# Performance work log

Measured on AMD Instinct MI355X. Metric: run time of the kernel, lower is better.

The kernel has to match this reference:

```python
import jax, jax.numpy as jnp
import numpy as np

T = 35        # points per voxel
D, H, W = 10, 400, 352  # voxel grid (KITTI car setting)
EPS = 1e-5    # BatchNorm eps


def setup_inputs() -> dict:
    key = jax.random.key(0)
    ks = jax.random.split(key, 10)
    K = 15000  # non-empty voxels in the frame
    feature = jax.random.normal(ks[0], (K, T, 7), jnp.float32)
    # realistic padding: each voxel has 5..35 valid points, rest zero
    npts = jax.random.randint(ks[1], (K,), 5, T + 1)
    valid = jnp.arange(T)[None, :] < npts[:, None]
    feature = feature * valid[:, :, None].astype(jnp.float32)
    c_b = jnp.zeros((K, 1), jnp.int32)
    c_d = jax.random.randint(ks[2], (K, 1), 0, D).astype(jnp.int32)
    c_h = jax.random.randint(ks[3], (K, 1), 0, H).astype(jnp.int32)
    c_w = jax.random.randint(ks[4], (K, 1), 0, W).astype(jnp.int32)
    coordinate = jnp.concatenate([c_b, c_d, c_h, c_w], axis=1)
    W1 = jax.random.normal(ks[5], (7, 16), jnp.float32) * 0.1
    b1 = jnp.zeros((16,), jnp.float32)
    g1 = jnp.ones((16,), jnp.float32)
    be1 = jnp.zeros((16,), jnp.float32)
    W2 = jax.random.normal(ks[6], (32, 64), jnp.float32) * 0.1
    b2 = jnp.zeros((64,), jnp.float32)
    g2 = jnp.ones((64,), jnp.float32)
    be2 = jnp.zeros((64,), jnp.float32)
    return {"feature": feature, "coordinate": coordinate, "bs": 1,
            "W1": W1, "b1": b1, "g1": g1, "be1": be1,
            "W2": W2, "b2": b2, "g2": g2, "be2": be2}


def _vfe(x, mask, Wm, b, g, be):
    # Linear + ReLU per point: [K, T, cin] -> [K, T, cmid]
    pw = jax.nn.relu(jnp.einsum('ktc,cd->ktd', x, Wm) + b)
    # BatchNorm1d (training mode): per-channel stats over (K, T), biased var
    mu = pw.mean(axis=(0, 1))
    var = pw.var(axis=(0, 1))
    pw = (pw - mu) * jax.lax.rsqrt(var + EPS) * g + be
    # max over points, broadcast-concat (VoxelNet VFE)
    agg = pw.max(axis=1, keepdims=True)               # [K, 1, cmid]
    cat = jnp.concatenate([pw, jnp.broadcast_to(agg, pw.shape)], axis=-1)
    return cat * mask  # mask padded points


def reference(feature, coordinate, bs, W1, b1, g1, be1, W2, b2, g2, be2):
    # mask: point is valid if its channel-wise max != 0 (as in original)
    vmax = feature.max(axis=2, keepdims=True)          # [K, T, 1]
    mask = (vmax != 0).astype(feature.dtype)
    x = _vfe(feature, mask, W1, b1, g1, be1)           # [K, T, 32]
    x = _vfe(x, mask, W2, b2, g2, be2)                 # [K, T, 128]
    voxelwise = x.max(axis=1)                          # [K, 128]
    # scatter into dense grid (sparse COO -> to_dense sums duplicates)
    out = jnp.zeros((bs, D, H, W, 128), feature.dtype)
    out = out.at[coordinate[:, 0], coordinate[:, 1],
                 coordinate[:, 2], coordinate[:, 3]].add(voxelwise)
    return out
```

## Files before the change

kernel.cpp:

```cpp
#include <hip/hip_runtime.h>
#include <math.h>

#define KVOX 15000
#define TP 35
#define CIN 7
#define CM1 16
#define CM2 64
#define NPTS (KVOX * TP)
#define DD 10
#define HH 400
#define WWID 352
#define NCELL (DD * HH * WWID)
#define EPSBN 1e-5f
#define NB1 256
#define NBV 3750

typedef float vfloat4 __attribute__((ext_vector_type(4)));
typedef int   vint4   __attribute__((ext_vector_type(4)));

#define NT4 (NCELL / 4)
__global__ __launch_bounds__(256) void init_kernel(vint4* __restrict__ table4)
{
    int i = blockIdx.x * 256 + threadIdx.x;
    table4[i] = (vint4){0x7FFFFFFF, 0x7FFFFFFF, 0x7FFFFFFF, 0x7FFFFFFF};
}

__global__ __launch_bounds__(256) void stats1_kernel(
    const float* __restrict__ feat, const int* __restrict__ coord,
    const float* __restrict__ W1, const float* __restrict__ b1,
    float* __restrict__ partial1, int* __restrict__ table)
{
    __shared__ float w1s[CIN * CM1];
    __shared__ float b1s[CM1];
    __shared__ float red[4][32];
    int tid = threadIdx.x;
    if (tid < CIN * CM1) w1s[tid] = W1[tid];
    if (tid < CM1) b1s[tid] = b1[tid];

    int g = blockIdx.x * 256 + tid;
    if (g < KVOX) {
        int cell = (coord[g * 4 + 1] * HH + coord[g * 4 + 2]) * WWID + coord[g * 4 + 3];
        atomicMin(&table[cell], g);
    }
    __syncthreads();

    float s[CM1], q[CM1];
#pragma unroll
    for (int c = 0; c < CM1; ++c) { s[c] = 0.f; q[c] = 0.f; }

    for (int i = blockIdx.x * 256 + tid; i < NPTS; i += NB1 * 256) {
        float f[CIN];
#pragma unroll
        for (int j = 0; j < CIN; ++j) f[j] = feat[(size_t)i * CIN + j];
#pragma unroll
        for (int c = 0; c < CM1; ++c) {
            float acc = b1s[c];
#pragma unroll
            for (int j = 0; j < CIN; ++j) acc = fmaf(f[j], w1s[j * CM1 + c], acc);
            float pw = fmaxf(acc, 0.f);
            s[c] += pw; q[c] += pw * pw;
        }
    }
#pragma unroll
    for (int c = 0; c < CM1; ++c) {
#pragma unroll
        for (int off = 32; off > 0; off >>= 1) {
            s[c] += __shfl_xor(s[c], off);
            q[c] += __shfl_xor(q[c], off);
        }
    }
    int wid = tid >> 6, lane = tid & 63;
    if (lane == 0) {
#pragma unroll
        for (int c = 0; c < CM1; ++c) { red[wid][c] = s[c]; red[wid][CM1 + c] = q[c]; }
    }
    __syncthreads();
    if (tid < 32)
        partial1[blockIdx.x * 32 + tid] =
            red[0][tid] + red[1][tid] + red[2][tid] + red[3][tid];
}

__global__ __launch_bounds__(256) void reduce1_kernel(
    const float* __restrict__ partial1, const float* __restrict__ g1,
    const float* __restrict__ be1, float* __restrict__ coef1)
{
    __shared__ float acc[8][32];
    __shared__ float tot[32];
    int tid = threadIdx.x;
    int c = tid & 31, part = tid >> 5;
    float v = 0.f;
    for (int b = part; b < NB1; b += 8) v += partial1[b * 32 + c];
    acc[part][c] = v;
    __syncthreads();
    if (tid < 32) {
        float t = 0.f;
#pragma unroll
        for (int p = 0; p < 8; ++p) t += acc[p][tid];
        tot[tid] = t;
    }
    __syncthreads();
    if (tid < CM1) {
        float inv = 1.f / (float)NPTS;
        float mu = tot[tid] * inv;
        float var = tot[CM1 + tid] * inv - mu * mu;
        float a = g1[tid] * rsqrtf(var + EPSBN);
        coef1[tid] = a;
        coef1[CM1 + tid] = be1[tid] - mu * a;
    }
}

__global__ __launch_bounds__(256) void vfe_once_kernel(
    const float* __restrict__ feat,
    const float* __restrict__ W1g, const float* __restrict__ b1g,
    const float* __restrict__ coef1,
    const float* __restrict__ W2g, const float* __restrict__ b2g,
    float* __restrict__ partial2,
    float* __restrict__ ext,
    int*   __restrict__ flags,
    vfloat4* __restrict__ compact4)
{
    __shared__ float sfeat[4][TP * CIN + 11];
    alignas(16) __shared__ float scat[4][TP * 32];
    __shared__ float smask[4][TP + 5];
    __shared__ float red2[4][2 * CM2];

    int tid = threadIdx.x, wid = tid >> 6, lane = tid & 63;
    int k = blockIdx.x * 4 + wid;
    int tg = lane >> 4, c1 = lane & 15;

    float w1r[CIN];
#pragma unroll
    for (int j = 0; j < CIN; ++j) w1r[j] = W1g[j * CM1 + c1];
    float b1r = b1g[c1];
    float a1r = coef1[c1], d1r = coef1[CM1 + c1];
    float w2r[32];
#pragma unroll
    for (int j = 0; j < 32; ++j) w2r[j] = W2g[j * CM2 + lane];
    float b2r = b2g[lane];

    float* F = sfeat[wid];
    float* CT = scat[wid];
    float* M = smask[wid];

    for (int i = lane; i < TP * CIN; i += 64)
        F[i] = feat[(size_t)k * (TP * CIN) + i];
    __syncthreads();

    float maxv = -INFINITY;
#pragma unroll
    for (int it = 0; it < 9; ++it) {
        int t = tg + 4 * it;
        if (t < TP) {
            float fv0 = F[t * CIN];
            float m7 = fv0;
            float acc = fmaf(fv0, w1r[0], b1r);
#pragma unroll
            for (int j = 1; j < CIN; ++j) {
                float fv = F[t * CIN + j];
                m7 = fmaxf(m7, fv);
                acc = fmaf(fv, w1r[j], acc);
            }
            float maskv = (m7 != 0.f) ? 1.f : 0.f;
            float pw = fmaxf(acc, 0.f);
            float bn = fmaf(pw, a1r, d1r);
            maxv = fmaxf(maxv, bn);
            CT[t * 32 + c1] = bn * maskv;
            if (c1 == 0) M[t] = maskv;
        }
    }
    maxv = fmaxf(maxv, __shfl_xor(maxv, 16));
    maxv = fmaxf(maxv, __shfl_xor(maxv, 32));
#pragma unroll
    for (int it = 0; it < 9; ++it) {
        int t = tg + 4 * it;
        if (t < TP) CT[t * 32 + 16 + c1] = maxv * M[t];
    }

    float s_acc = 0.f, q_acc = 0.f;
    float pwmax_v = -INFINITY, pwmin_v = INFINITY;
    float pwmax_a = -INFINITY, pwmin_a = INFINITY;
    float mmin = 1.f;
    for (int t = 0; t < TP; ++t) {
        const float4* r4 = reinterpret_cast<const float4*>(&CT[t * 32]);
        float acc0 = b2r, acc1 = 0.f;
#pragma unroll
        for (int i = 0; i < 8; i += 2) {
            float4 va = r4[i], vb = r4[i + 1];
            acc0 = fmaf(va.x, w2r[4 * i + 0], acc0);
            acc0 = fmaf(va.y, w2r[4 * i + 1], acc0);
            acc0 = fmaf(va.z, w2r[4 * i + 2], acc0);
            acc0 = fmaf(va.w, w2r[4 * i + 3], acc0);
            acc1 = fmaf(vb.x, w2r[4 * i + 4], acc1);
            acc1 = fmaf(vb.y, w2r[4 * i + 5], acc1);
            acc1 = fmaf(vb.z, w2r[4 * i + 6], acc1);
            acc1 = fmaf(vb.w, w2r[4 * i + 7], acc1);
        }
        float pw = fmaxf(acc0 + acc1, 0.f);
        s_acc += pw; q_acc += pw * pw;
        float mk = M[t];
        mmin = fminf(mmin, mk);
        pwmax_a = fmaxf(pwmax_a, pw);
        pwmin_a = fminf(pwmin_a, pw);
        pwmax_v = fmaxf(pwmax_v, (mk != 0.f) ? pw : -INFINITY);
        pwmin_v = fminf(pwmin_v, (mk != 0.f) ? pw : INFINITY);
    }

    float* E = ext + (size_t)k * 256;
    E[lane] = pwmax_v; E[64 + lane] = pwmin_v;
    E[128 + lane] = pwmax_a; E[192 + lane] = pwmin_a;
    if (lane == 0) flags[k] = (mmin == 0.f) ? 1 : 0;

    red2[wid][lane] = s_acc;
    red2[wid][CM2 + lane] = q_acc;
    __syncthreads();
    if (tid < 2 * CM2)
        partial2[(size_t)blockIdx.x * (2 * CM2) + tid] =
            red2[0][tid] + red2[1][tid] + red2[2][tid] + red2[3][tid];

    if (tid < 128)
        compact4[(size_t)blockIdx.x * 128 + tid] = (vfloat4){0.f, 0.f, 0.f, 0.f};
}

__global__ __launch_bounds__(256) void reduce2_kernel(
    const float* __restrict__ partial2, const float* __restrict__ g2,
    const float* __restrict__ be2, float* __restrict__ coef2)
{
    __shared__ float sred[4][2];
    int c = blockIdx.x;
    int tid = threadIdx.x;
    float s = 0.f, q = 0.f;
    for (int r = tid; r < NBV; r += 256) {
        s += partial2[(size_t)r * 128 + c];
        q += partial2[(size_t)r * 128 + CM2 + c];
    }
#pragma unroll
    for (int off = 32; off > 0; off >>= 1) {
        s += __shfl_xor(s, off);
        q += __shfl_xor(q, off);
    }
    int wid = tid >> 6;
    if ((tid & 63) == 0) { sred[wid][0] = s; sred[wid][1] = q; }
    __syncthreads();
    if (tid == 0) {
        float S = sred[0][0] + sred[1][0] + sred[2][0] + sred[3][0];
        float Q = sred[0][1] + sred[1][1] + sred[2][1] + sred[3][1];
        float inv = 1.f / (float)NPTS;
        float mu = S * inv;
        float var = Q * inv - mu * mu;
        float a = g2[c] * rsqrtf(var + EPSBN);
        coef2[c] = a;
        coef2[CM2 + c] = be2[c] - mu * a;
    }
}

__global__ __launch_bounds__(256) void finalize_kernel(
    const float* __restrict__ ext, const int* __restrict__ flags,
    const int* __restrict__ coord, const float* __restrict__ coef2,
    const int* __restrict__ table, float* __restrict__ compact)
{
    int tid = threadIdx.x;
    int k = blockIdx.x * 2 + (tid >> 7);
    int sub = tid & 127;
    int c = sub & 63, half = sub >> 6;
    float a = coef2[c], d = coef2[CM2 + c];
    const float* E = ext + (size_t)k * 256 + half * 128;
    float hi = E[c], lo = E[64 + c];
    float val = (a >= 0.f) ? fmaf(a, hi, d) : fmaf(a, lo, d);
    if (flags[k]) val = fmaxf(val, 0.f);
    int cell = (coord[k * 4 + 1] * HH + coord[k * 4 + 2]) * WWID + coord[k * 4 + 3];
    int w = table[cell];
    atomicAdd(&compact[(size_t)w * 128 + sub], val);
}

#define NBW (NCELL * 32 / 256)
__global__ __launch_bounds__(256) void write_kernel(
    vfloat4* __restrict__ out, const int* __restrict__ table,
    const vfloat4* __restrict__ compact4)
{
    int i = blockIdx.x * 256 + threadIdx.x;
    int cell = i >> 5;
    int w = table[cell];
    vfloat4 v = {0.f, 0.f, 0.f, 0.f};
    if (w < KVOX) v = compact4[w * 32 + (i & 31)];
    out[i] = v;
}

extern "C" void kernel_launch(void* const* d_in, const int* in_sizes, int n_in,
                              void* d_out, int out_size, void* d_ws, size_t ws_size,
                              hipStream_t stream)
{
    const float* feat = (const float*)d_in[0];
    const int*   coord = (const int*)d_in[1];
    const float* W1  = (const float*)d_in[3];
    const float* b1  = (const float*)d_in[4];
    const float* g1  = (const float*)d_in[5];
    const float* be1 = (const float*)d_in[6];
    const float* W2  = (const float*)d_in[7];
    const float* b2  = (const float*)d_in[8];
    const float* g2  = (const float*)d_in[9];
    const float* be2 = (const float*)d_in[10];
    float* out = (float*)d_out;

    int*   table    = (int*)d_ws;
    float* compact  = (float*)d_ws + NCELL;
    float* ext      = compact + (size_t)KVOX * 128;
    float* partial1 = ext + (size_t)KVOX * 256;
    float* partial2 = partial1 + NB1 * 32;
    int*   flags    = (int*)(partial2 + NBV * 128);
    float* coef1    = (float*)(flags + KVOX);
    float* coef2    = coef1 + 32;

    init_kernel<<<NT4 / 256, 256, 0, stream>>>((vint4*)table);
    stats1_kernel<<<NB1, 256, 0, stream>>>(feat, coord, W1, b1, partial1, table);
    reduce1_kernel<<<1, 256, 0, stream>>>(partial1, g1, be1, coef1);
    vfe_once_kernel<<<NBV, 256, 0, stream>>>(feat, W1, b1, coef1, W2, b2,
                                             partial2, ext, flags,
                                             (vfloat4*)compact);
    reduce2_kernel<<<CM2, 256, 0, stream>>>(partial2, g2, be2, coef2);
    finalize_kernel<<<KVOX / 2, 256, 0, stream>>>(ext, flags, coord, coef2,
                                                  table, compact);
    write_kernel<<<NBW, 256, 0, stream>>>((vfloat4*)out, table, (vfloat4*)compact);
}
```

Before: 836.4 us.

## Use bf16 MFMA for second VFE layer and grid-stride the dense write

The second VFE linear layer (32->64 per point) now runs on MFMA 16x16x32 bf16 instructions instead of scalar FMAs. Layer-1 outputs are stored to shared memory as bf16 with padded rows, and the per-channel statistics and max/min are reduced across lanes with shuffles. The dense output write kernel becomes a grid-stride loop over a fixed 2048 blocks instead of one block per 256 vectors. bf16 rounding of activations and weights adds precision loss relative to the fp32 reference.

```diff
diff --git a/kernel.cpp b/kernel.cpp
--- a/kernel.cpp
+++ b/kernel.cpp
@@ -14,9 +14,19 @@
 #define EPSBN 1e-5f
 #define NB1 256
 #define NBV 3750
+#define NBW 2048
 
 typedef float vfloat4 __attribute__((ext_vector_type(4)));
 typedef int   vint4   __attribute__((ext_vector_type(4)));
+typedef short bf16x8  __attribute__((ext_vector_type(8)));
+typedef float f32x4   __attribute__((ext_vector_type(4)));
+
+__device__ inline unsigned short f2b(float x)
+{
+    unsigned int u = __float_as_uint(x);
+    unsigned int r = (u + 0x7FFFu + ((u >> 16) & 1u)) >> 16;
+    return (unsigned short)r;
+}
 
 #define NT4 (NCELL / 4)
 __global__ __launch_bounds__(256) void init_kernel(vint4* __restrict__ table4)
@@ -119,9 +129,9 @@
     int*   __restrict__ flags,
     vfloat4* __restrict__ compact4)
 {
-    __shared__ float sfeat[4][TP * CIN + 11];
-    alignas(16) __shared__ float scat[4][TP * 32];
-    __shared__ float smask[4][TP + 5];
+    __shared__ float sfeat[4][256];
+    __shared__ vint4 sct4[4][288];
+    __shared__ float smask[4][48];
     __shared__ float red2[4][2 * CM2];
 
     int tid = threadIdx.x, wid = tid >> 6, lane = tid & 63;
@@ -133,18 +143,30 @@
     for (int j = 0; j < CIN; ++j) w1r[j] = W1g[j * CM1 + c1];
     float b1r = b1g[c1];
     float a1r = coef1[c1], d1r = coef1[CM1 + c1];
-    float w2r[32];
-#pragma unroll
-    for (int j = 0; j < 32; ++j) w2r[j] = W2g[j * CM2 + lane];
-    float b2r = b2g[lane];
+
+    bf16x8 bfr[4];
+    float bias[4];
+#pragma unroll
+    for (int nt = 0; nt < 4; ++nt) {
+        bias[nt] = b2g[nt * 16 + c1];
+#pragma unroll
+        for (int j = 0; j < 8; ++j)
+            bfr[nt][j] = (short)f2b(W2g[(tg * 8 + j) * 64 + nt * 16 + c1]);
+    }
 
     float* F = sfeat[wid];
-    float* CT = scat[wid];
+    unsigned short* CT = (unsigned short*)sct4[wid];
     float* M = smask[wid];
 
     for (int i = lane; i < TP * CIN; i += 64)
         F[i] = feat[(size_t)k * (TP * CIN) + i];
-    __syncthreads();
+    {
+        vint4 z = {0, 0, 0, 0};
+        vint4* pz = (vint4*)(CT + 35 * 48);
+        pz[lane] = z;
+        if (lane < 14) pz[64 + lane] = z;
+        if (lane < 13) M[35 + lane] = 0.f;
+    }
 
     float maxv = -INFINITY;
 #pragma unroll
@@ -164,7 +186,7 @@
             float pw = fmaxf(acc, 0.f);
             float bn = fmaf(pw, a1r, d1r);
             maxv = fmaxf(maxv, bn);
-            CT[t * 32 + c1] = bn * maskv;
+            CT[t * 48 + c1] = f2b(bn * maskv);
             if (c1 == 0) M[t] = maskv;
         }
     }
@@ -173,45 +195,81 @@
 #pragma unroll
     for (int it = 0; it < 9; ++it) {
         int t = tg + 4 * it;
-        if (t < TP) CT[t * 32 + 16 + c1] = maxv * M[t];
-    }
-
-    float s_acc = 0.f, q_acc = 0.f;
-    float pwmax_v = -INFINITY, pwmin_v = INFINITY;
-    float pwmax_a = -INFINITY, pwmin_a = INFINITY;
+        if (t < TP) CT[t * 48 + 16 + c1] = f2b(maxv * M[t]);
+    }
+
+    f32x4 acc[3][4] = {};
+#pragma unroll
+    for (int mt = 0; mt < 3; ++mt) {
+        bf16x8 a = ((bf16x8*)sct4[wid])[(16 * mt + c1) * 6 + tg];
+#pragma unroll
+        for (int nt = 0; nt < 4; ++nt)
+            acc[mt][nt] = __builtin_amdgcn_mfma_f32_16x16x32_bf16(
+                a, bfr[nt], acc[mt][nt], 0, 0, 0);
+    }
+
+    float s[4] = {0.f, 0.f, 0.f, 0.f}, q[4] = {0.f, 0.f, 0.f, 0.f};
+    float mxv[4], mnv[4], mxa[4], mna[4];
+#pragma unroll
+    for (int nt = 0; nt < 4; ++nt) {
+        mxv[nt] = -INFINITY; mnv[nt] = INFINITY;
+        mxa[nt] = -INFINITY; mna[nt] = INFINITY;
+    }
     float mmin = 1.f;
-    for (int t = 0; t < TP; ++t) {
-        const float4* r4 = reinterpret_cast<const float4*>(&CT[t * 32]);
-        float acc0 = b2r, acc1 = 0.f;
-#pragma unroll
-        for (int i = 0; i < 8; i += 2) {
-            float4 va = r4[i], vb = r4[i + 1];
-            acc0 = fmaf(va.x, w2r[4 * i + 0], acc0);
-            acc0 = fmaf(va.y, w2r[4 * i + 1], acc0);
-            acc0 = fmaf(va.z, w2r[4 * i + 2], acc0);
-            acc0 = fmaf(va.w, w2r[4 * i + 3], acc0);
-            acc1 = fmaf(vb.x, w2r[4 * i + 4], acc1);
-            acc1 = fmaf(vb.y, w2r[4 * i + 5], acc1);
-            acc1 = fmaf(vb.z, w2r[4 * i + 6], acc1);
-            acc1 = fmaf(vb.w, w2r[4 * i + 7], acc1);
+#pragma unroll
+    for (int mt = 0; mt < 3; ++mt) {
+#pragma unroll
+        for (int r = 0; r < 4; ++r) {
+            int row = 16 * mt + tg * 4 + r;
+            bool live = row < TP;
+            float mk = M[row];
+            if (live) mmin = fminf(mmin, mk);
+            bool vld = live && (mk != 0.f);
+#pragma unroll
+            for (int nt = 0; nt < 4; ++nt) {
+                float pw = fmaxf(acc[mt][nt][r] + bias[nt], 0.f);
+                if (live) {
+                    s[nt] += pw; q[nt] += pw * pw;
+                    mxa[nt] = fmaxf(mxa[nt], pw);
+                    mna[nt] = fminf(mna[nt], pw);
+                }
+                if (vld) {
+                    mxv[nt] = fmaxf(mxv[nt], pw);
+                    mnv[nt] = fminf(mnv[nt], pw);
+                }
+            }
         }
-        float pw = fmaxf(acc0 + acc1, 0.f);
-        s_acc += pw; q_acc += pw * pw;
-        float mk = M[t];
-        mmin = fminf(mmin, mk);
-        pwmax_a = fmaxf(pwmax_a, pw);
-        pwmin_a = fminf(pwmin_a, pw);
-        pwmax_v = fmaxf(pwmax_v, (mk != 0.f) ? pw : -INFINITY);
-        pwmin_v = fminf(pwmin_v, (mk != 0.f) ? pw : INFINITY);
-    }
+    }
+#pragma unroll
+    for (int nt = 0; nt < 4; ++nt) {
+        s[nt] += __shfl_xor(s[nt], 16);  s[nt] += __shfl_xor(s[nt], 32);
+        q[nt] += __shfl_xor(q[nt], 16);  q[nt] += __shfl_xor(q[nt], 32);
+        mxv[nt] = fmaxf(mxv[nt], __shfl_xor(mxv[nt], 16));
+        mxv[nt] = fmaxf(mxv[nt], __shfl_xor(mxv[nt], 32));
+        mnv[nt] = fminf(mnv[nt], __shfl_xor(mnv[nt], 16));
+        mnv[nt] = fminf(mnv[nt], __shfl_xor(mnv[nt], 32));
+        mxa[nt] = fmaxf(mxa[nt], __shfl_xor(mxa[nt], 16));
+        mxa[nt] = fmaxf(mxa[nt], __shfl_xor(mxa[nt], 32));
+        mna[nt] = fminf(mna[nt], __shfl_xor(mna[nt], 16));
+        mna[nt] = fminf(mna[nt], __shfl_xor(mna[nt], 32));
+    }
+    mmin = fminf(mmin, __shfl_xor(mmin, 16));
+    mmin = fminf(mmin, __shfl_xor(mmin, 32));
+
+    float o_mxv = tg == 0 ? mxv[0] : tg == 1 ? mxv[1] : tg == 2 ? mxv[2] : mxv[3];
+    float o_mnv = tg == 0 ? mnv[0] : tg == 1 ? mnv[1] : tg == 2 ? mnv[2] : mnv[3];
+    float o_mxa = tg == 0 ? mxa[0] : tg == 1 ? mxa[1] : tg == 2 ? mxa[2] : mxa[3];
+    float o_mna = tg == 0 ? mna[0] : tg == 1 ? mna[1] : tg == 2 ? mna[2] : mna[3];
+    float o_s   = tg == 0 ? s[0]   : tg == 1 ? s[1]   : tg == 2 ? s[2]   : s[3];
+    float o_q   = tg == 0 ? q[0]   : tg == 1 ? q[1]   : tg == 2 ? q[2]   : q[3];
 
     float* E = ext + (size_t)k * 256;
-    E[lane] = pwmax_v; E[64 + lane] = pwmin_v;
-    E[128 + lane] = pwmax_a; E[192 + lane] = pwmin_a;
+    E[lane] = o_mxv; E[64 + lane] = o_mnv;
+    E[128 + lane] = o_mxa; E[192 + lane] = o_mna;
     if (lane == 0) flags[k] = (mmin == 0.f) ? 1 : 0;
 
-    red2[wid][lane] = s_acc;
-    red2[wid][CM2 + lane] = q_acc;
+    red2[wid][lane] = o_s;
+    red2[wid][CM2 + lane] = o_q;
     __syncthreads();
     if (tid < 2 * CM2)
         partial2[(size_t)blockIdx.x * (2 * CM2) + tid] =
@@ -272,17 +330,19 @@
     atomicAdd(&compact[(size_t)w * 128 + sub], val);
 }
 
-#define NBW (NCELL * 32 / 256)
 __global__ __launch_bounds__(256) void write_kernel(
     vfloat4* __restrict__ out, const int* __restrict__ table,
     const vfloat4* __restrict__ compact4)
 {
-    int i = blockIdx.x * 256 + threadIdx.x;
-    int cell = i >> 5;
-    int w = table[cell];
-    vfloat4 v = {0.f, 0.f, 0.f, 0.f};
-    if (w < KVOX) v = compact4[w * 32 + (i & 31)];
-    out[i] = v;
+    const int total = NCELL * 32;
+    int stride = NBW * 256;
+    for (int i = blockIdx.x * 256 + threadIdx.x; i < total; i += stride) {
+        int cell = i >> 5;
+        int w = table[cell];
+        vfloat4 v = {0.f, 0.f, 0.f, 0.f};
+        if (w < KVOX) v = compact4[w * 32 + (i & 31)];
+        out[i] = v;
+    }
 }
 
 extern "C" void kernel_launch(void* const* d_in, const int* in_sizes, int n_in,
```

New measurement: 789.0 us. 5.7% less time.
